# Optimization experiments

Measured on AMD Instinct MI355X. Metric: run time of the kernel, lower is better.

Reference implementation:

```python
import jax, jax.numpy as jnp
import numpy as np

N = 50000
E = 1600000
D_IN = 768
NHID = 256
NCLASS = 2


def _spmm(rows, cols, vals, dense):
    # out[i] = sum_{e: rows[e]==i} vals[e] * dense[cols[e]]
    return jax.ops.segment_sum(vals[:, None] * dense[cols], rows, num_segments=N)


def _att_fusion(x1, x2, x3, w):
    # a: [N,3] -> abs -> softmax over the 3 branches
    a = jnp.abs(jnp.concatenate([x1, x2, x3], axis=-1) @ w)
    a = jax.nn.softmax(a, axis=-1)  # [N,3]
    x = jnp.stack([x1, x2, x3], axis=-1)  # [N,H,3]
    return jnp.sum(x * a[:, None, :], axis=-1)  # [N,H]


def setup_inputs() -> dict:
    key = jax.random.key(0)
    ks = jax.random.split(key, 24)

    def u(k, shape, fan):
        s = 1.0 / np.sqrt(fan)
        return jax.random.uniform(k, shape, jnp.float32, -s, s)

    inp = {
        "x": jax.random.normal(ks[0], (N, D_IN), jnp.float32),
        "adj_rows": jax.random.randint(ks[1], (E,), 0, N, jnp.int32),
        "adj_cols": jax.random.randint(ks[2], (E,), 0, N, jnp.int32),
        "adj_vals": jax.random.uniform(ks[3], (E,), jnp.float32),
        "s_rows": jax.random.randint(ks[4], (E,), 0, N, jnp.int32),
        "s_cols": jax.random.randint(ks[5], (E,), 0, N, jnp.int32),
        "s_vals": jax.random.uniform(ks[6], (E,), jnp.float32),
        "W1r1": u(ks[7], (D_IN, NHID), NHID),
        "b1r1": u(ks[8], (NHID,), NHID),
        "W1r2": u(ks[9], (D_IN, NHID), NHID),
        "b1r2": u(ks[10], (NHID,), NHID),
        "mlp1_W": u(ks[11], (D_IN, NHID), D_IN),
        "mlp1_b": u(ks[12], (NHID,), D_IN),
        "af1_w": u(ks[13], (3 * NHID, 3), 3 * NHID),
        "W2r1": u(ks[14], (NHID, NCLASS), NCLASS),
        "b2r1": u(ks[15], (NCLASS,), NCLASS),
        "W2r2": u(ks[16], (NHID, NCLASS), NCLASS),
        "b2r2": u(ks[17], (NCLASS,), NCLASS),
        "mlp2_W": u(ks[18], (NHID, NCLASS), NHID),
        "mlp2_b": u(ks[19], (NCLASS,), NHID),
    }
    return inp


def reference(x, adj_rows, adj_cols, adj_vals, s_rows, s_cols, s_vals,
              W1r1, b1r1, W1r2, b1r2, mlp1_W, mlp1_b, af1_w,
              W2r1, b2r1, W2r2, b2r2, mlp2_W, mlp2_b):
    # dropout in eval mode -> identity
    # layer 1: two sparse GCN branches + tanh MLP branch, attention fused
    x_r1 = _spmm(adj_rows, adj_cols, adj_vals, x @ W1r1) + b1r1
    x_r2 = _spmm(s_rows, s_cols, s_vals, x @ W1r2) + b1r2
    x_1 = jnp.tanh(x @ mlp1_W + mlp1_b)
    x1 = _att_fusion(x_r1, x_r2, x_1, af1_w)  # [N, NHID]

    # layer 2: summed branches
    y_r1 = _spmm(adj_rows, adj_cols, adj_vals, x1 @ W2r1) + b2r1
    y_r2 = _spmm(s_rows, s_cols, s_vals, x1 @ W2r2) + b2r2
    y_1 = jnp.tanh(x1 @ mlp2_W + mlp2_b)
    return y_r2 + y_r1 + y_1  # [N, NCLASS]
```

## Files before the change

kernel.cpp:

```cpp
#include <hip/hip_runtime.h>
#include <hip/hip_bf16.h>

#define NN 50000
#define EE 1600000
#define DIN 768
#define NH 256

typedef unsigned short u16;
typedef unsigned int u32;

typedef __attribute__((ext_vector_type(8))) short short8;
typedef __attribute__((ext_vector_type(4))) float f32x4;

__device__ __forceinline__ float bf2f(u16 u) {
  union { u32 i; float f; } x; x.i = ((u32)u) << 16; return x.f;
}
__device__ __forceinline__ u16 f2bf(float f) {
  union { float f; u32 u; } x; x.f = f;
  u32 r = x.u + 0x7fff + ((x.u >> 16) & 1);
  return (u16)(r >> 16);
}

__global__ __launch_bounds__(256) void prep_kernel(
    const float* __restrict__ X, u16* __restrict__ Xb,
    const int* __restrict__ rA, const int* __restrict__ rB,
    int* __restrict__ cntA, int* __restrict__ cntB,
    const float* __restrict__ Wa, const float* __restrict__ Wb,
    const float* __restrict__ Wc, u16* __restrict__ Wt) {
  int b = blockIdx.x;
  if (b < 37500) {
    size_t idx = (size_t)b * 256 + threadIdx.x;
    float4 v = reinterpret_cast<const float4*>(X)[idx];
    ushort4 o;
    o.x = f2bf(v.x); o.y = f2bf(v.y); o.z = f2bf(v.z); o.w = f2bf(v.w);
    reinterpret_cast<ushort4*>(Xb)[idx] = o;
  } else if (b < 50000) {
    int e = (b - 37500) * 256 + threadIdx.x;
    if (e < EE) atomicAdd(&cntA[rA[e]], 1);
    else        atomicAdd(&cntB[rB[e - EE]], 1);
  } else {
    int idx = (b - 50000) * 256 + threadIdx.x;
    int n = idx / DIN, k = idx - n * DIN;
    const float* W = (n < 256) ? Wa : (n < 512) ? Wb : Wc;
    Wt[idx] = f2bf(W[(size_t)k * NH + (n & 255)]);
  }
}

__global__ __launch_bounds__(256) void scan1(int* __restrict__ cntA, int* __restrict__ rsA,
                                             int* __restrict__ cntB, int* __restrict__ rsB,
                                             int* __restrict__ bsum) {
  int* cnt = (blockIdx.y == 0) ? cntA : cntB;
  int* rs  = (blockIdx.y == 0) ? rsA  : rsB;
  int* bs  = bsum + blockIdx.y * 98;
  __shared__ int wsum[4];
  int t = threadIdx.x, lane = t & 63, wid = t >> 6;
  int i0 = blockIdx.x * 512 + 2 * t;
  int v0 = (i0 < NN) ? cnt[i0] : 0;
  int v1 = (i0 + 1 < NN) ? cnt[i0 + 1] : 0;
  int s = v0 + v1;
  int sc = s;
#pragma unroll
  for (int off = 1; off < 64; off <<= 1) {
    int tv = __shfl_up(sc, off, 64);
    if (lane >= off) sc += tv;
  }
  if (lane == 63) wsum[wid] = sc;
  __syncthreads();
  int woff = 0;
  for (int w = 0; w < wid; ++w) woff += wsum[w];
  int excl = woff + sc - s;
  if (i0 < NN)     { cnt[i0] = excl;          rs[i0 + 1] = excl + v0; }
  if (i0 + 1 < NN) { cnt[i0 + 1] = excl + v0; rs[i0 + 2] = excl + v0 + v1; }
  if (t == 255) bs[blockIdx.x] = woff + sc;
  if (blockIdx.x == 0 && t == 0) rs[0] = 0;
}

__global__ __launch_bounds__(512) void scan3(int* __restrict__ cntA, int* __restrict__ rsA,
                                             int* __restrict__ cntB, int* __restrict__ rsB,
                                             const int* __restrict__ bsum) {
  int* cnt = (blockIdx.y == 0) ? cntA : cntB;
  int* rs  = (blockIdx.y == 0) ? rsA  : rsB;
  __shared__ int bs[98];
  if (threadIdx.x < 98) bs[threadIdx.x] = bsum[blockIdx.y * 98 + threadIdx.x];
  __syncthreads();
  int off = 0;
  for (int k = 0; k < blockIdx.x; ++k) off += bs[k];
  int i = blockIdx.x * 512 + threadIdx.x;
  if (i < NN) { cnt[i] += off; rs[i + 1] += off; }
}

#define TM 128
#define TN 128
#define TK 32
#define GEMM_BLKS 2346
#define SCAT_BLKS 3125
#define TOT_BLKS (GEMM_BLKS + SCAT_BLKS)

__device__ __forceinline__ void gload16(const u16* g, u16* lds) {
  __builtin_amdgcn_global_load_lds((const __attribute__((address_space(1))) unsigned int*)g,
                                   (__attribute__((address_space(3))) unsigned int*)lds, 16, 0, 0);
}

__global__ __launch_bounds__(256) void gemm_scatter(
    const u16* __restrict__ Xb, const u16* __restrict__ Wt, const float* __restrict__ mlp1_b,
    u16* __restrict__ H1, u16* __restrict__ H2, u16* __restrict__ T,
    const int* __restrict__ rA, const int* __restrict__ cA, const float* __restrict__ vA,
    const int* __restrict__ rB, const int* __restrict__ cB, const float* __restrict__ vB,
    int* __restrict__ curA, u32* __restrict__ edgeA,
    int* __restrict__ curB, u32* __restrict__ edgeB) {
  __shared__ u16 As[TM * TK];
  __shared__ u16 Bs[TN * TK];

  const int b = blockIdx.x;
  const int lo = (b * GEMM_BLKS) / TOT_BLKS;
  const int hi = ((b + 1) * GEMM_BLKS) / TOT_BLKS;

  if (hi > lo) {
    const int gid = lo;
    const int tid = threadIdx.x;
    const int lane = tid & 63;
    const int w = tid >> 6;
    const int n0 = (gid % 6) * TN;
    const int m0 = (gid / 6) * TM;
    const int wm = w >> 1, wn = w & 1;

    f32x4 acc[4][4] = {};

    const int r_l = lane >> 2;
    const int kcp = lane & 3;
    const int r16 = lane & 15;
    const int kcl = lane >> 4;

    for (int k0 = 0; k0 < DIN; k0 += TK) {
#pragma unroll
      for (int q = 0; q < 2; ++q) {
        int row = w * 32 + q * 16 + r_l;
        int kc = kcp ^ ((row >> 1) & 3);
        int gr = m0 + row; if (gr >= NN) gr = NN - 1;
        gload16(Xb + (size_t)gr * DIN + k0 + kc * 8, &As[(w * 32 + q * 16) * TK]);
        gload16(Wt + (size_t)(n0 + row) * DIN + k0 + kc * 8, &Bs[(w * 32 + q * 16) * TK]);
      }
      __syncthreads();

      short8 aF[4], bF[4];
#pragma unroll
      for (int i = 0; i < 4; ++i) {
        int m = wm * 64 + i * 16 + r16;
        aF[i] = *reinterpret_cast<const short8*>(&As[m * TK + (kcl ^ ((m >> 1) & 3)) * 8]);
        int n = wn * 64 + i * 16 + r16;
        bF[i] = *reinterpret_cast<const short8*>(&Bs[n * TK + (kcl ^ ((n >> 1) & 3)) * 8]);
      }
#pragma unroll
      for (int i = 0; i < 4; ++i)
#pragma unroll
        for (int j = 0; j < 4; ++j)
          acc[i][j] = __builtin_amdgcn_mfma_f32_16x16x32_bf16(aF[i], bF[j], acc[i][j], 0, 0, 0);
      __syncthreads();
    }

    const int bsel = n0 >> 8;
    u16* O = (bsel == 0) ? H1 : (bsel == 1) ? H2 : T;
    const int act = (bsel == 2);
    const int cb = n0 & 255;
    const int rq = lane >> 4;
#pragma unroll
    for (int i = 0; i < 4; ++i) {
#pragma unroll
      for (int rr = 0; rr < 4; ++rr) {
        int grow = m0 + wm * 64 + i * 16 + rq * 4 + rr;
        if (grow >= NN) continue;
#pragma unroll
        for (int j = 0; j < 4; ++j) {
          int c = cb + wn * 64 + j * 16 + r16;
          float v = acc[i][j][rr];
          if (act) v = tanhf(v + mlp1_b[c]);
          O[(size_t)grow * NH + c] = f2bf(v);
        }
      }
    }
  } else {
    const int sid = b - lo;
    const int base = sid * 1024 + threadIdx.x;
    int rws[4]; u32 pks[4];
#pragma unroll
    for (int q = 0; q < 4; ++q) {
      int e = base + q * 256;
      rws[q] = (e < EE) ? rA[e] : rB[e - EE];
    }
#pragma unroll
    for (int q = 0; q < 4; ++q) {
      int e = base + q * 256;
      if (e < EE) pks[q] = (u32)(u16)cA[e] | ((u32)f2bf(vA[e]) << 16);
      else        pks[q] = (u32)(u16)cB[e - EE] | ((u32)f2bf(vB[e - EE]) << 16);
    }
#pragma unroll
    for (int q = 0; q < 4; ++q) {
      int e = base + q * 256;
      if (e < EE) { int p = atomicAdd(&curA[rws[q]], 1); edgeA[p] = pks[q]; }
      else        { int p = atomicAdd(&curB[rws[q]], 1); edgeB[p] = pks[q]; }
    }
  }
}

__global__ __launch_bounds__(256) void spmm_fuse(
    const int* __restrict__ rsA, const u32* __restrict__ edgeA,
    const u16* __restrict__ H1, const float* __restrict__ b1,
    const int* __restrict__ rsB, const u32* __restrict__ edgeB,
    const u16* __restrict__ H2, const float* __restrict__ b2,
    const u16* __restrict__ T, const float* __restrict__ afw,
    const float* __restrict__ W2r1, const float* __restrict__ W2r2,
    const float* __restrict__ mlpW, const float* __restrict__ mlpb,
    float* __restrict__ Z1, float* __restrict__ Z2, float* __restrict__ Y1) {
  __shared__ float w[DIN * 3];
  __shared__ float w1[NH * 2], w2[NH * 2], wmm[NH * 2];
  int tid = threadIdx.x;
  for (int i = tid; i < DIN * 3; i += 256) w[i] = afw[i];
  for (int i = tid; i < NH * 2; i += 256) { w1[i] = W2r1[i]; w2[i] = W2r2[i]; wmm[i] = mlpW[i]; }
  __syncthreads();

  int lane = tid & 63, wv = tid >> 6;
  int n = blockIdx.x * 4 + wv;
  int h0 = (lane & 31) * 8;
  int eg = lane >> 5;

  float ac1[8] = {}, ac2[8] = {};
  {
    int s = rsA[n], e = rsA[n + 1];
    int i = s + eg;
    for (; i + 14 < e; i += 16) {
      u32 ew[8];
#pragma unroll
      for (int q = 0; q < 8; ++q) ew[q] = edgeA[i + 2 * q];
      short8 hv[8];
#pragma unroll
      for (int q = 0; q < 8; ++q)
        hv[q] = *reinterpret_cast<const short8*>(H1 + (size_t)(ew[q] & 0xFFFF) * NH + h0);
#pragma unroll
      for (int q = 0; q < 8; ++q) {
        float f = bf2f((u16)(ew[q] >> 16));
#pragma unroll
        for (int j = 0; j < 8; ++j) ac1[j] += f * bf2f((u16)hv[q][j]);
      }
    }
    for (; i + 6 < e; i += 8) {
      u32 ew[4];
#pragma unroll
      for (int q = 0; q < 4; ++q) ew[q] = edgeA[i + 2 * q];
      short8 hv[4];
#pragma unroll
      for (int q = 0; q < 4; ++q)
        hv[q] = *reinterpret_cast<const short8*>(H1 + (size_t)(ew[q] & 0xFFFF) * NH + h0);
#pragma unroll
      for (int q = 0; q < 4; ++q) {
        float f = bf2f((u16)(ew[q] >> 16));
#pragma unroll
        for (int j = 0; j < 8; ++j) ac1[j] += f * bf2f((u16)hv[q][j]);
      }
    }
    for (; i < e; i += 2) {
      u32 e0 = edgeA[i];
      short8 v0 = *reinterpret_cast<const short8*>(H1 + (size_t)(e0 & 0xFFFF) * NH + h0);
      float f0 = bf2f((u16)(e0 >> 16));
#pragma unroll
      for (int j = 0; j < 8; ++j) ac1[j] += f0 * bf2f((u16)v0[j]);
    }
  }
  {
    int s = rsB[n], e = rsB[n + 1];
    int i = s + eg;
    for (; i + 14 < e; i += 16) {
      u32 ew[8];
#pragma unroll
      for (int q = 0; q < 8; ++q) ew[q] = edgeB[i + 2 * q];
      short8 hv[8];
#pragma unroll
      for (int q = 0; q < 8; ++q)
        hv[q] = *reinterpret_cast<const short8*>(H2 + (size_t)(ew[q] & 0xFFFF) * NH + h0);
#pragma unroll
      for (int q = 0; q < 8; ++q) {
        float f = bf2f((u16)(ew[q] >> 16));
#pragma unroll
        for (int j = 0; j < 8; ++j) ac2[j] += f * bf2f((u16)hv[q][j]);
      }
    }
    for (; i + 6 < e; i += 8) {
      u32 ew[4];
#pragma unroll
      for (int q = 0; q < 4; ++q) ew[q] = edgeB[i + 2 * q];
      short8 hv[4];
#pragma unroll
      for (int q = 0; q < 4; ++q)
        hv[q] = *reinterpret_cast<const short8*>(H2 + (size_t)(ew[q] & 0xFFFF) * NH + h0);
#pragma unroll
      for (int q = 0; q < 4; ++q) {
        float f = bf2f((u16)(ew[q] >> 16));
#pragma unroll
        for (int j = 0; j < 8; ++j) ac2[j] += f * bf2f((u16)hv[q][j]);
      }
    }
    for (; i < e; i += 2) {
      u32 e0 = edgeB[i];
      short8 v0 = *reinterpret_cast<const short8*>(H2 + (size_t)(e0 & 0xFFFF) * NH + h0);
      float f0 = bf2f((u16)(e0 >> 16));
#pragma unroll
      for (int j = 0; j < 8; ++j) ac2[j] += f0 * bf2f((u16)v0[j]);
    }
  }
#pragma unroll
  for (int j = 0; j < 8; ++j) {
    ac1[j] += __shfl_xor(ac1[j], 32, 64);
    ac2[j] += __shfl_xor(ac2[j], 32, 64);
  }

  float r1[8], r2[8], t8[8];
  {
    float4 bA0 = *reinterpret_cast<const float4*>(b1 + h0);
    float4 bA1 = *reinterpret_cast<const float4*>(b1 + h0 + 4);
    float4 bB0 = *reinterpret_cast<const float4*>(b2 + h0);
    float4 bB1 = *reinterpret_cast<const float4*>(b2 + h0 + 4);
    float bbA[8] = {bA0.x, bA0.y, bA0.z, bA0.w, bA1.x, bA1.y, bA1.z, bA1.w};
    float bbB[8] = {bB0.x, bB0.y, bB0.z, bB0.w, bB1.x, bB1.y, bB1.z, bB1.w};
    short8 tv = *reinterpret_cast<const short8*>(T + (size_t)n * NH + h0);
#pragma unroll
    for (int j = 0; j < 8; ++j) {
      r1[j] = ac1[j] + bbA[j];
      r2[j] = ac2[j] + bbB[j];
      t8[j] = bf2f((u16)tv[j]);
    }
  }

  float l0 = 0.f, l1 = 0.f, l2 = 0.f;
#pragma unroll
  for (int k = 0; k < 8; ++k) {
    int h = h0 + k;
    l0 += r1[k] * w[h * 3 + 0] + r2[k] * w[(NH + h) * 3 + 0] + t8[k] * w[(2 * NH + h) * 3 + 0];
    l1 += r1[k] * w[h * 3 + 1] + r2[k] * w[(NH + h) * 3 + 1] + t8[k] * w[(2 * NH + h) * 3 + 1];
    l2 += r1[k] * w[h * 3 + 2] + r2[k] * w[(NH + h) * 3 + 2] + t8[k] * w[(2 * NH + h) * 3 + 2];
  }
#pragma unroll
  for (int off = 16; off > 0; off >>= 1) {
    l0 += __shfl_xor(l0, off, 64);
    l1 += __shfl_xor(l1, off, 64);
    l2 += __shfl_xor(l2, off, 64);
  }
  l0 = fabsf(l0); l1 = fabsf(l1); l2 = fabsf(l2);
  float mx = fmaxf(l0, fmaxf(l1, l2));
  float e0 = expf(l0 - mx), e1 = expf(l1 - mx), e2 = expf(l2 - mx);
  float inv = 1.f / (e0 + e1 + e2);
  float s0 = e0 * inv, s1 = e1 * inv, s2 = e2 * inv;

  float p10 = 0.f, p11 = 0.f, p20 = 0.f, p21 = 0.f, p30 = 0.f, p31 = 0.f;
#pragma unroll
  for (int k = 0; k < 8; ++k) {
    int h = h0 + k;
    float xv = s0 * r1[k] + s1 * r2[k] + s2 * t8[k];
    p10 += xv * w1[h * 2 + 0]; p11 += xv * w1[h * 2 + 1];
    p20 += xv * w2[h * 2 + 0]; p21 += xv * w2[h * 2 + 1];
    p30 += xv * wmm[h * 2 + 0]; p31 += xv * wmm[h * 2 + 1];
  }
#pragma unroll
  for (int off = 16; off > 0; off >>= 1) {
    p10 += __shfl_xor(p10, off, 64); p11 += __shfl_xor(p11, off, 64);
    p20 += __shfl_xor(p20, off, 64); p21 += __shfl_xor(p21, off, 64);
    p30 += __shfl_xor(p30, off, 64); p31 += __shfl_xor(p31, off, 64);
  }
  if (lane == 0) {
    Z1[n * 2 + 0] = p10; Z1[n * 2 + 1] = p11;
    Z2[n * 2 + 0] = p20; Z2[n * 2 + 1] = p21;
    Y1[n * 2 + 0] = tanhf(p30 + mlpb[0]);
    Y1[n * 2 + 1] = tanhf(p31 + mlpb[1]);
  }
}

__global__ __launch_bounds__(256) void spmm2_final(
    const int* __restrict__ rsA, const u32* __restrict__ edgeA,
    const int* __restrict__ rsB, const u32* __restrict__ edgeB,
    const float* __restrict__ Z1, const float* __restrict__ Z2, const float* __restrict__ Y1,
    const float* __restrict__ b2r1, const float* __restrict__ b2r2,
    float* __restrict__ out) {
  int tid = threadIdx.x;
  int lane = tid & 63, wave = tid >> 6;
  int n = blockIdx.x * 4 + wave;
  int half = lane >> 5, l32 = lane & 31;
  const int* rs = half ? rsB : rsA;
  const u32* edge = half ? edgeB : edgeA;
  const float* Z = half ? Z2 : Z1;
  float a0 = 0.f, a1 = 0.f;
  int s = rs[n], e = rs[n + 1];
  int i = s + l32;
  for (; i + 32 < e; i += 64) {
    u32 e0 = edge[i], e1 = edge[i + 32];
    float v0 = bf2f((u16)(e0 >> 16)), v1 = bf2f((u16)(e1 >> 16));
    float2 z0 = *reinterpret_cast<const float2*>(Z + (e0 & 0xFFFF) * 2);
    float2 z1 = *reinterpret_cast<const float2*>(Z + (e1 & 0xFFFF) * 2);
    a0 += v0 * z0.x + v1 * z1.x;
    a1 += v0 * z0.y + v1 * z1.y;
  }
  if (i < e) {
    u32 e0 = edge[i];
    float v0 = bf2f((u16)(e0 >> 16));
    float2 z0 = *reinterpret_cast<const float2*>(Z + (e0 & 0xFFFF) * 2);
    a0 += v0 * z0.x; a1 += v0 * z0.y;
  }
#pragma unroll
  for (int off = 16; off > 0; off >>= 1) {
    a0 += __shfl_xor(a0, off, 64);
    a1 += __shfl_xor(a1, off, 64);
  }
  float bsum0 = __shfl(a0, 32, 64);
  float bsum1 = __shfl(a1, 32, 64);
  if (lane == 0) {
    out[n * 2 + 0] = (a0 + b2r1[0]) + (bsum0 + b2r2[0]) + Y1[n * 2 + 0];
    out[n * 2 + 1] = (a1 + b2r1[1]) + (bsum1 + b2r2[1]) + Y1[n * 2 + 1];
  }
}

extern "C" void kernel_launch(void* const* d_in, const int* in_sizes, int n_in,
                              void* d_out, int out_size, void* d_ws, size_t ws_size,
                              hipStream_t stream) {
  const float* x        = (const float*)d_in[0];
  const int*   adj_rows = (const int*)d_in[1];
  const int*   adj_cols = (const int*)d_in[2];
  const float* adj_vals = (const float*)d_in[3];
  const int*   s_rows   = (const int*)d_in[4];
  const int*   s_cols   = (const int*)d_in[5];
  const float* s_vals   = (const float*)d_in[6];
  const float* W1r1     = (const float*)d_in[7];
  const float* b1r1     = (const float*)d_in[8];
  const float* W1r2     = (const float*)d_in[9];
  const float* b1r2     = (const float*)d_in[10];
  const float* mlp1_W   = (const float*)d_in[11];
  const float* mlp1_b   = (const float*)d_in[12];
  const float* af1_w    = (const float*)d_in[13];
  const float* W2r1     = (const float*)d_in[14];
  const float* b2r1     = (const float*)d_in[15];
  const float* W2r2     = (const float*)d_in[16];
  const float* b2r2     = (const float*)d_in[17];
  const float* mlp2_W   = (const float*)d_in[18];
  const float* mlp2_b   = (const float*)d_in[19];
  float* out = (float*)d_out;

  char* p = (char*)d_ws;
  auto alloc = [&](size_t b) { char* r = p; p += (b + 255) & ~(size_t)255; return r; };

  char* xb_region = alloc((size_t)NN * DIN * 2);
  u16* Xb = (u16*)xb_region;
  float* Z1 = (float*)xb_region;
  float* Z2 = (float*)(xb_region + (size_t)NN * 2 * 4);
  float* Y1 = (float*)(xb_region + (size_t)NN * 4 * 4);

  u16* H1 = (u16*)alloc((size_t)NN * NH * 2);
  u16* H2 = (u16*)alloc((size_t)NN * NH * 2);
  u16* T  = (u16*)alloc((size_t)NN * NH * 2);
  u16* Wt = (u16*)alloc((size_t)DIN * DIN * 2);
  int* rsA   = (int*)alloc((size_t)(NN + 1) * 4);
  int* curA  = (int*)alloc((size_t)NN * 4);
  u32* edgeA = (u32*)alloc((size_t)EE * 4);
  int* rsB   = (int*)alloc((size_t)(NN + 1) * 4);
  int* curB  = (int*)alloc((size_t)NN * 4);
  u32* edgeB = (u32*)alloc((size_t)EE * 4);
  int* bsum  = (int*)alloc(2 * 98 * 4);

  hipMemsetAsync(curA, 0, (size_t)NN * 4, stream);
  hipMemsetAsync(curB, 0, (size_t)NN * 4, stream);
  prep_kernel<<<52304, 256, 0, stream>>>(x, Xb, adj_rows, s_rows, curA, curB,
                                         W1r1, W1r2, mlp1_W, Wt);

  dim3 gsc(98, 2);
  scan1<<<gsc, 256, 0, stream>>>(curA, rsA, curB, rsB, bsum);
  scan3<<<dim3(98, 2), 512, 0, stream>>>(curA, rsA, curB, rsB, bsum);

  gemm_scatter<<<TOT_BLKS, 256, 0, stream>>>(Xb, Wt, mlp1_b, H1, H2, T,
                                             adj_rows, adj_cols, adj_vals,
                                             s_rows, s_cols, s_vals,
                                             curA, edgeA, curB, edgeB);

  spmm_fuse<<<NN / 4, 256, 0, stream>>>(rsA, edgeA, H1, b1r1,
                                        rsB, edgeB, H2, b1r2,
                                        T, af1_w, W2r1, W2r2, mlp2_W, mlp2_b,
                                        Z1, Z2, Y1);

  spmm2_final<<<NN / 4, 256, 0, stream>>>(rsA, edgeA, rsB, edgeB,
                                          Z1, Z2, Y1, b2r1, b2r2, out);
}
```

Before: 865.2 us.

## Use nontemporal loads/stores, widen scatter per block, unroll spmm2, merge memsets

Marks streaming loads and stores (X conversion, edge lists, GEMM outputs, CSR edge arrays) as nontemporal so they bypass or are demoted in cache. Each scatter block now handles 2048 edges instead of 1024, with bounds guards for the tail. The spmm2 inner loop is unrolled four-wide to raise memory-level parallelism, and the two counter memsets are merged into one. Nontemporal stores of H1/H2/T may hurt because those arrays are re-read by gathers immediately after.

Result: no change. 875.1 us (+1.1%).

```diff
diff --git a/kernel.cpp b/kernel.cpp
--- a/kernel.cpp
+++ b/kernel.cpp
@@ -11,6 +11,7 @@
 
 typedef __attribute__((ext_vector_type(8))) short short8;
 typedef __attribute__((ext_vector_type(4))) float f32x4;
+typedef __attribute__((ext_vector_type(4))) unsigned short us4;
 
 __device__ __forceinline__ float bf2f(u16 u) {
   union { u32 i; float f; } x; x.i = ((u32)u) << 16; return x.f;
@@ -30,14 +31,14 @@
   int b = blockIdx.x;
   if (b < 37500) {
     size_t idx = (size_t)b * 256 + threadIdx.x;
-    float4 v = reinterpret_cast<const float4*>(X)[idx];
-    ushort4 o;
+    f32x4 v = __builtin_nontemporal_load(reinterpret_cast<const f32x4*>(X) + idx);
+    us4 o;
     o.x = f2bf(v.x); o.y = f2bf(v.y); o.z = f2bf(v.z); o.w = f2bf(v.w);
-    reinterpret_cast<ushort4*>(Xb)[idx] = o;
+    reinterpret_cast<us4*>(Xb)[idx] = o;
   } else if (b < 50000) {
     int e = (b - 37500) * 256 + threadIdx.x;
-    if (e < EE) atomicAdd(&cntA[rA[e]], 1);
-    else        atomicAdd(&cntB[rB[e - EE]], 1);
+    if (e < EE) atomicAdd(&cntA[__builtin_nontemporal_load(rA + e)], 1);
+    else        atomicAdd(&cntB[__builtin_nontemporal_load(rB + e - EE)], 1);
   } else {
     int idx = (b - 50000) * 256 + threadIdx.x;
     int n = idx / DIN, k = idx - n * DIN;
@@ -93,7 +94,7 @@
 #define TN 128
 #define TK 32
 #define GEMM_BLKS 2346
-#define SCAT_BLKS 3125
+#define SCAT_BLKS 1563
 #define TOT_BLKS (GEMM_BLKS + SCAT_BLKS)
 
 __device__ __forceinline__ void gload16(const u16* g, u16* lds) {
@@ -174,30 +175,36 @@
           int c = cb + wn * 64 + j * 16 + r16;
           float v = acc[i][j][rr];
           if (act) v = tanhf(v + mlp1_b[c]);
-          O[(size_t)grow * NH + c] = f2bf(v);
+          __builtin_nontemporal_store(f2bf(v), O + (size_t)grow * NH + c);
         }
       }
     }
   } else {
     const int sid = b - lo;
-    const int base = sid * 1024 + threadIdx.x;
-    int rws[4]; u32 pks[4];
-#pragma unroll
-    for (int q = 0; q < 4; ++q) {
+    const int base = sid * 2048 + threadIdx.x;
+    int rws[8]; u32 pks[8];
+#pragma unroll
+    for (int q = 0; q < 8; ++q) {
       int e = base + q * 256;
-      rws[q] = (e < EE) ? rA[e] : rB[e - EE];
-    }
-#pragma unroll
-    for (int q = 0; q < 4; ++q) {
+      if (e < EE)            rws[q] = __builtin_nontemporal_load(rA + e);
+      else if (e < 2 * EE)   rws[q] = __builtin_nontemporal_load(rB + e - EE);
+      else                   rws[q] = -1;
+    }
+#pragma unroll
+    for (int q = 0; q < 8; ++q) {
       int e = base + q * 256;
-      if (e < EE) pks[q] = (u32)(u16)cA[e] | ((u32)f2bf(vA[e]) << 16);
-      else        pks[q] = (u32)(u16)cB[e - EE] | ((u32)f2bf(vB[e - EE]) << 16);
-    }
-#pragma unroll
-    for (int q = 0; q < 4; ++q) {
+      if (e < EE)
+        pks[q] = (u32)(u16)__builtin_nontemporal_load(cA + e)
+               | ((u32)f2bf(__builtin_nontemporal_load(vA + e)) << 16);
+      else if (e < 2 * EE)
+        pks[q] = (u32)(u16)__builtin_nontemporal_load(cB + e - EE)
+               | ((u32)f2bf(__builtin_nontemporal_load(vB + e - EE)) << 16);
+    }
+#pragma unroll
+    for (int q = 0; q < 8; ++q) {
       int e = base + q * 256;
-      if (e < EE) { int p = atomicAdd(&curA[rws[q]], 1); edgeA[p] = pks[q]; }
-      else        { int p = atomicAdd(&curB[rws[q]], 1); edgeB[p] = pks[q]; }
+      if (e < EE)          { int p = atomicAdd(&curA[rws[q]], 1); __builtin_nontemporal_store(pks[q], edgeA + p); }
+      else if (e < 2 * EE) { int p = atomicAdd(&curB[rws[q]], 1); __builtin_nontemporal_store(pks[q], edgeB + p); }
     }
   }
 }
@@ -230,7 +237,7 @@
     for (; i + 14 < e; i += 16) {
       u32 ew[8];
 #pragma unroll
-      for (int q = 0; q < 8; ++q) ew[q] = edgeA[i + 2 * q];
+      for (int q = 0; q < 8; ++q) ew[q] = __builtin_nontemporal_load(edgeA + i + 2 * q);
       short8 hv[8];
 #pragma unroll
       for (int q = 0; q < 8; ++q)
@@ -245,7 +252,7 @@
     for (; i + 6 < e; i += 8) {
       u32 ew[4];
 #pragma unroll
-      for (int q = 0; q < 4; ++q) ew[q] = edgeA[i + 2 * q];
+      for (int q = 0; q < 4; ++q) ew[q] = __builtin_nontemporal_load(edgeA + i + 2 * q);
       short8 hv[4];
 #pragma unroll
       for (int q = 0; q < 4; ++q)
@@ -258,7 +265,7 @@
       }
     }
     for (; i < e; i += 2) {
-      u32 e0 = edgeA[i];
+      u32 e0 = __builtin_nontemporal_load(edgeA + i);
       short8 v0 = *reinterpret_cast<const short8*>(H1 + (size_t)(e0 & 0xFFFF) * NH + h0);
       float f0 = bf2f((u16)(e0 >> 16));
 #pragma unroll
@@ -271,7 +278,7 @@
     for (; i + 14 < e; i += 16) {
       u32 ew[8];
 #pragma unroll
-      for (int q = 0; q < 8; ++q) ew[q] = edgeB[i + 2 * q];
+      for (int q = 0; q < 8; ++q) ew[q] = __builtin_nontemporal_load(edgeB + i + 2 * q);
       short8 hv[8];
 #pragma unroll
       for (int q = 0; q < 8; ++q)
@@ -286,7 +293,7 @@
     for (; i + 6 < e; i += 8) {
       u32 ew[4];
 #pragma unroll
-      for (int q = 0; q < 4; ++q) ew[q] = edgeB[i + 2 * q];
+      for (int q = 0; q < 4; ++q) ew[q] = __builtin_nontemporal_load(edgeB + i + 2 * q);
       short8 hv[4];
 #pragma unroll
       for (int q = 0; q < 4; ++q)
@@ -299,7 +306,7 @@
       }
     }
     for (; i < e; i += 2) {
-      u32 e0 = edgeB[i];
+      u32 e0 = __builtin_nontemporal_load(edgeB + i);
       short8 v0 = *reinterpret_cast<const short8*>(H2 + (size_t)(e0 & 0xFFFF) * NH + h0);
       float f0 = bf2f((u16)(e0 >> 16));
 #pragma unroll
@@ -388,16 +395,21 @@
   float a0 = 0.f, a1 = 0.f;
   int s = rs[n], e = rs[n + 1];
   int i = s + l32;
-  for (; i + 32 < e; i += 64) {
-    u32 e0 = edge[i], e1 = edge[i + 32];
-    float v0 = bf2f((u16)(e0 >> 16)), v1 = bf2f((u16)(e1 >> 16));
-    float2 z0 = *reinterpret_cast<const float2*>(Z + (e0 & 0xFFFF) * 2);
-    float2 z1 = *reinterpret_cast<const float2*>(Z + (e1 & 0xFFFF) * 2);
-    a0 += v0 * z0.x + v1 * z1.x;
-    a1 += v0 * z0.y + v1 * z1.y;
-  }
-  if (i < e) {
-    u32 e0 = edge[i];
+  for (; i + 96 < e; i += 128) {
+    u32 ew[4];
+#pragma unroll
+    for (int q = 0; q < 4; ++q) ew[q] = __builtin_nontemporal_load(edge + i + 32 * q);
+    float2 z[4];
+#pragma unroll
+    for (int q = 0; q < 4; ++q) z[q] = *reinterpret_cast<const float2*>(Z + (ew[q] & 0xFFFF) * 2);
+#pragma unroll
+    for (int q = 0; q < 4; ++q) {
+      float v = bf2f((u16)(ew[q] >> 16));
+      a0 += v * z[q].x; a1 += v * z[q].y;
+    }
+  }
+  for (; i < e; i += 32) {
+    u32 e0 = __builtin_nontemporal_load(edge + i);
     float v0 = bf2f((u16)(e0 >> 16));
     float2 z0 = *reinterpret_cast<const float2*>(Z + (e0 & 0xFFFF) * 2);
     a0 += v0 * z0.x; a1 += v0 * z0.y;
@@ -453,16 +465,16 @@
   u16* H2 = (u16*)alloc((size_t)NN * NH * 2);
   u16* T  = (u16*)alloc((size_t)NN * NH * 2);
   u16* Wt = (u16*)alloc((size_t)DIN * DIN * 2);
+  int* curz  = (int*)alloc((size_t)2 * NN * 4);
+  int* curA  = curz;
+  int* curB  = curz + NN;
   int* rsA   = (int*)alloc((size_t)(NN + 1) * 4);
-  int* curA  = (int*)alloc((size_t)NN * 4);
   u32* edgeA = (u32*)alloc((size_t)EE * 4);
   int* rsB   = (int*)alloc((size_t)(NN + 1) * 4);
-  int* curB  = (int*)alloc((size_t)NN * 4);
   u32* edgeB = (u32*)alloc((size_t)EE * 4);
   int* bsum  = (int*)alloc(2 * 98 * 4);
 
-  hipMemsetAsync(curA, 0, (size_t)NN * 4, stream);
-  hipMemsetAsync(curB, 0, (size_t)NN * 4, stream);
+  (void)hipMemsetAsync(curz, 0, (size_t)2 * NN * 4, stream);
   prep_kernel<<<52304, 256, 0, stream>>>(x, Xb, adj_rows, s_rows, curA, curB,
                                          W1r1, W1r2, mlp1_W, Wt);
 
```
